# Kernel tuning notes

Measured on AMD Instinct MI355X. Metric: run time of the kernel, lower is better.

The kernel has to match this reference:

```python
import jax, jax.numpy as jnp
import numpy as np

N_NODES = 100000
N_EDGES = 1600000
N_GRAPHS = 64


def _sage(x, src, dst, Wl, bl, Wr):
    # SAGEConv (mean aggr): out = lin_l(mean_j x_j) + lin_r(x_i)
    msg = x[src]                                             # [E, F] gather
    s = jax.ops.segment_sum(msg, dst, num_segments=N_NODES)  # [N, F]
    cnt = jax.ops.segment_sum(jnp.ones((msg.shape[0],), x.dtype), dst,
                              num_segments=N_NODES)[:, None]
    mean = jnp.where(cnt > 0, s / jnp.maximum(cnt, 1.0), 0.0)
    return mean @ Wl + bl + x @ Wr


def setup_inputs() -> dict:
    key = jax.random.key(0)
    ks = jax.random.split(key, 12)
    sc = lambda f: 1.0 / np.sqrt(f)
    inp = {
        'x':   jax.random.normal(ks[0], (N_NODES, 32), jnp.float32),
        'Wl0': jax.random.normal(ks[1], (32, 64), jnp.float32) * sc(32),
        'bl0': jnp.zeros((64,), jnp.float32),
        'Wr0': jax.random.normal(ks[2], (32, 64), jnp.float32) * sc(32),
        'Wl1': jax.random.normal(ks[3], (64, 64), jnp.float32) * sc(64),
        'bl1': jnp.zeros((64,), jnp.float32),
        'Wr1': jax.random.normal(ks[4], (64, 64), jnp.float32) * sc(64),
        'Wl2': jax.random.normal(ks[5], (64, 64), jnp.float32) * sc(64),
        'bl2': jnp.zeros((64,), jnp.float32),
        'Wr2': jax.random.normal(ks[6], (64, 64), jnp.float32) * sc(64),
        'W_out': jax.random.normal(ks[7], (64, 8), jnp.float32) * sc(64),
        'b_out': jnp.zeros((8,), jnp.float32),
        'edge_index': jax.random.randint(ks[8], (2, N_EDGES), 0, N_NODES, jnp.int32),
        'batch': jnp.sort(jax.random.randint(ks[9], (N_NODES,), 0, N_GRAPHS, jnp.int32)),
    }
    return inp


def reference(x, Wl0, bl0, Wr0, Wl1, bl1, Wr1, Wl2, bl2, Wr2,
              W_out, b_out, edge_index, batch):
    src, dst = edge_index[0], edge_index[1]
    h = _sage(x, src, dst, Wl0, bl0, Wr0)
    h = _sage(h, src, dst, Wl1, bl1, Wr1)
    h = _sage(h, src, dst, Wl2, bl2, Wr2)
    pooled = jax.ops.segment_max(h, batch, num_segments=N_GRAPHS)  # [G, 64]
    logits = pooled @ W_out + b_out
    return jax.nn.log_softmax(logits, axis=-1)
```

## Files before the change

### kernel.cpp

```cpp
#include <hip/hip_runtime.h>
#include <math.h>
#include <stdint.h>

#define N_NODES 100000
#define N_EDGES 1600000
#define N_GRAPHS 64

#define BSH 9
#define NBKT 196
#define NCHUNK 256
#define EPC 6250
#define FLAT (NBKT * NCHUNK)


typedef __attribute__((ext_vector_type(8))) short bf16x8;
typedef __attribute__((ext_vector_type(8))) unsigned short u16x8;
typedef __attribute__((ext_vector_type(4))) float f32x4;

#define WT0L 0
#define WT0R 2048
#define WT1L 4096
#define WT1R 8192
#define WT2L 12288
#define WT2R 16384

__device__ __forceinline__ void atomicMaxFloat(float* addr, float val) {
    if (val >= 0.0f) {
        atomicMax((int*)addr, __float_as_int(val));
    } else {
        atomicMin((unsigned int*)addr, __float_as_uint(val));
    }
}

__device__ __forceinline__ unsigned short f2bf(float f) {
    unsigned u = __float_as_uint(f);
    unsigned r = (u + 0x7FFFu + ((u >> 16) & 1u)) >> 16;
    return (unsigned short)r;
}
__device__ __forceinline__ float bf2f(unsigned short b) {
    return __uint_as_float(((unsigned)b) << 16);
}

__global__ __launch_bounds__(256) void k_prep(
    const float* __restrict__ x, unsigned short* __restrict__ xhi,
    const int* __restrict__ batch, int* __restrict__ gstart,
    float* __restrict__ pooled,
    const float* __restrict__ Wl0, const float* __restrict__ Wr0,
    const float* __restrict__ Wl1, const float* __restrict__ Wr1,
    const float* __restrict__ Wl2, const float* __restrict__ Wr2,
    unsigned short* __restrict__ WT,
    const int* __restrict__ dst, int* __restrict__ S) {
    __shared__ int h[NBKT];
    int i = blockIdx.x * blockDim.x + threadIdx.x;

    if (i < N_NODES * 32 / 8) {
        int base = i * 8;
        const float4* xp = (const float4*)(x + base);
        float4 a = xp[0], b = xp[1];
        u16x8 o;
        o[0] = f2bf(a.x); o[1] = f2bf(a.y); o[2] = f2bf(a.z); o[3] = f2bf(a.w);
        o[4] = f2bf(b.x); o[5] = f2bf(b.y); o[6] = f2bf(b.z); o[7] = f2bf(b.w);
        *(u16x8*)(xhi + base) = o;
    }
    if (i < N_GRAPHS * 64) pooled[i] = -INFINITY;
    if (i < N_NODES) {
        int b = batch[i];
        if (i == 0) {
            for (int g = 0; g <= b; ++g) gstart[g] = 0;
        } else {
            int pb = batch[i - 1];
            for (int g = pb + 1; g <= b; ++g) gstart[g] = i;
        }
        if (i == N_NODES - 1) {
            for (int g = b + 1; g <= N_GRAPHS; ++g) gstart[g] = N_NODES;
        }
    }
    if (i < 2560) {
        const float* Wsrc; int wofs, KW, local;
        if (i < 256)       { Wsrc = Wl0; wofs = WT0L; KW = 32; local = i; }
        else if (i < 512)  { Wsrc = Wr0; wofs = WT0R; KW = 32; local = i - 256; }
        else if (i < 1024) { Wsrc = Wl1; wofs = WT1L; KW = 64; local = i - 512; }
        else if (i < 1536) { Wsrc = Wr1; wofs = WT1R; KW = 64; local = i - 1024; }
        else if (i < 2048) { Wsrc = Wl2; wofs = WT2L; KW = 64; local = i - 1536; }
        else               { Wsrc = Wr2; wofs = WT2R; KW = 64; local = i - 2048; }
        int e = local * 8;
        int colw = e / KW, k0 = e % KW;
        u16x8 o;
#pragma unroll
        for (int j = 0; j < 8; ++j) o[j] = f2bf(Wsrc[(size_t)(k0 + j) * 64 + colw]);
        *(u16x8*)(WT + wofs + e) = o;
    }
    if (blockIdx.x < NCHUNK) {
        for (int q = threadIdx.x; q < NBKT; q += 256) h[q] = 0;
        __syncthreads();
        int c = blockIdx.x;
        int e0 = c * EPC;
        for (int e = e0 + threadIdx.x; e < e0 + EPC; e += 256)
            atomicAdd(&h[dst[e] >> BSH], 1);
        __syncthreads();
        for (int q = threadIdx.x; q < NBKT; q += 256) S[q * NCHUNK + c] = h[q];
    }
}

__global__ __launch_bounds__(1024) void k_rscan(int* __restrict__ S) {
    __shared__ int part[1024];
    int t = threadIdx.x;
    const int seg = (FLAT + 1023) / 1024;
    int lo = t * seg;
    int hi = lo + seg; if (hi > FLAT) hi = FLAT;
    int s = 0;
    for (int i = lo; i < hi; ++i) s += S[i];
    part[t] = s;
    __syncthreads();
    for (int off = 1; off < 1024; off <<= 1) {
        int add = (t >= off) ? part[t - off] : 0;
        __syncthreads();
        part[t] += add;
        __syncthreads();
    }
    int ex = (t > 0) ? part[t - 1] : 0;
    if (t == 1023) S[FLAT] = part[1023];
    int run = ex;
    for (int i = lo; i < hi; ++i) { int v = S[i]; S[i] = run; run += v; }
}

__global__ __launch_bounds__(256) void k_rscatter(
    const int* __restrict__ src, const int* __restrict__ dst,
    const int* __restrict__ S, unsigned int* __restrict__ pairs) {
    __shared__ int ofs[NBKT];
    __shared__ int cnt[NBKT];
    int c = blockIdx.x;
    for (int i = threadIdx.x; i < NBKT; i += 256) {
        ofs[i] = S[i * NCHUNK + c];
        cnt[i] = 0;
    }
    __syncthreads();
    int e0 = c * EPC;
    for (int e = e0 + threadIdx.x; e < e0 + EPC; e += 256) {
        int d = dst[e];
        int b = d >> BSH;
        int r = atomicAdd(&cnt[b], 1);
        pairs[ofs[b] + r] = ((unsigned)(d & 511) << 17) | (unsigned)src[e];
    }
}

__global__ __launch_bounds__(256) void k_rbuild(
    const unsigned int* __restrict__ pairs, const int* __restrict__ S,
    int* __restrict__ row_ptr, int* __restrict__ col) {
    __shared__ int ncnt[512];
    __shared__ int nofs[512];
    __shared__ int part[256];
    int b = blockIdx.x;
    int t = threadIdx.x;
    int base = S[b * NCHUNK];
    int next = (b == NBKT - 1) ? S[FLAT] : S[(b + 1) * NCHUNK];
    int count = next - base;
    int nodeBase = b << BSH;

    ncnt[2 * t] = 0; ncnt[2 * t + 1] = 0;
    __syncthreads();
    for (int i = t; i < count; i += 256)
        atomicAdd(&ncnt[pairs[base + i] >> 17], 1);
    __syncthreads();
    int v0 = ncnt[2 * t], v1 = ncnt[2 * t + 1];
    part[t] = v0 + v1;
    __syncthreads();
    for (int off = 1; off < 256; off <<= 1) {
        int add = (t >= off) ? part[t - off] : 0;
        __syncthreads();
        part[t] += add;
        __syncthreads();
    }
    int ex = (t > 0) ? part[t - 1] : 0;
    nofs[2 * t] = ex;
    nofs[2 * t + 1] = ex + v0;
    ncnt[2 * t] = 0; ncnt[2 * t + 1] = 0;
    __syncthreads();
    for (int i = t; i < 512; i += 256) {
        int node = nodeBase + i;
        if (node < N_NODES) row_ptr[node] = base + nofs[i];
    }
    if (b == 0 && t == 0) row_ptr[N_NODES] = N_EDGES;
    for (int i = t; i < count; i += 256) {
        unsigned p = pairs[base + i];
        int li = p >> 17;
        int r = atomicAdd(&ncnt[li], 1);
        col[base + nofs[li] + r] = (int)(p & 0x1FFFFu);
    }
}

template <int KM, bool XBF, int KX, int XS, int OM>
__global__ __launch_bounds__(256) void k_sage_fused(
    const unsigned short* __restrict__ ghb,
    const float* x,
    const unsigned short* xhi, const unsigned short* xlo,
    const int* __restrict__ row_ptr, const int* __restrict__ col,
    const unsigned short* __restrict__ WTl,
    const float* __restrict__ bl,
    const unsigned short* __restrict__ WTr,
    unsigned short* ohi, unsigned short* olo) {
    __shared__ float amean[2][16][KM + 4];

    int lane = threadIdx.x & 63;
    int wid  = threadIdx.x >> 6;
    int sl   = wid >> 1;
    int half = wid & 1;
    int strip = blockIdx.x * 2 + sl;
    int row0 = strip * 16;

    {
        constexpr int G = (KM == 64) ? 4 : 8;
        constexpr int LPR = 64 / G;
        int g  = lane / LPR;
        int fq = lane % LPR;
        int nodeBase = row0 + half * 8;
        int rp = row_ptr[nodeBase + (lane < 8 ? lane : 8)];

        for (int i = 0; i < 8; ++i) {
            int start = __shfl(rp, i);
            int end   = __shfl(rp, i + 1);
            float s0 = 0.0f, s1 = 0.0f, s2 = 0.0f, s3 = 0.0f;

            for (int eb = start; eb < end; eb += 64) {
                int n = end - eb; if (n > 64) n = 64;
                int c = (eb + lane < end) ? col[eb + lane] : 0;
                int j = 0;
                for (; j + 4 * G - 1 < n; j += 4 * G) {
                    int cA = __shfl(c, j + g);
                    int cB = __shfl(c, j + G + g);
                    int cC = __shfl(c, j + 2 * G + g);
                    int cD = __shfl(c, j + 3 * G + g);
                    ushort4 vA = *(const ushort4*)(ghb + (size_t)cA * KM + fq * 4);
                    ushort4 vB = *(const ushort4*)(ghb + (size_t)cB * KM + fq * 4);
                    ushort4 vC = *(const ushort4*)(ghb + (size_t)cC * KM + fq * 4);
                    ushort4 vD = *(const ushort4*)(ghb + (size_t)cD * KM + fq * 4);
                    s0 += (bf2f(vA.x) + bf2f(vB.x)) + (bf2f(vC.x) + bf2f(vD.x));
                    s1 += (bf2f(vA.y) + bf2f(vB.y)) + (bf2f(vC.y) + bf2f(vD.y));
                    s2 += (bf2f(vA.z) + bf2f(vB.z)) + (bf2f(vC.z) + bf2f(vD.z));
                    s3 += (bf2f(vA.w) + bf2f(vB.w)) + (bf2f(vC.w) + bf2f(vD.w));
                }
                for (; j + 2 * G - 1 < n; j += 2 * G) {
                    int cA = __shfl(c, j + g);
                    int cB = __shfl(c, j + G + g);
                    ushort4 vA = *(const ushort4*)(ghb + (size_t)cA * KM + fq * 4);
                    ushort4 vB = *(const ushort4*)(ghb + (size_t)cB * KM + fq * 4);
                    s0 += bf2f(vA.x) + bf2f(vB.x);
                    s1 += bf2f(vA.y) + bf2f(vB.y);
                    s2 += bf2f(vA.z) + bf2f(vB.z);
                    s3 += bf2f(vA.w) + bf2f(vB.w);
                }
                for (; j + G - 1 < n; j += G) {
                    int cA = __shfl(c, j + g);
                    ushort4 vA = *(const ushort4*)(ghb + (size_t)cA * KM + fq * 4);
                    s0 += bf2f(vA.x);
                    s1 += bf2f(vA.y);
                    s2 += bf2f(vA.z);
                    s3 += bf2f(vA.w);
                }
                if (j < n) {
                    int idx = j + g;
                    bool valid = idx < n;
                    int cA = __shfl(c, valid ? idx : 0);
                    ushort4 vA = *(const ushort4*)(ghb + (size_t)cA * KM + fq * 4);
                    if (valid) {
                        s0 += bf2f(vA.x);
                        s1 += bf2f(vA.y);
                        s2 += bf2f(vA.z);
                        s3 += bf2f(vA.w);
                    }
                }
            }
#pragma unroll
            for (int m = LPR; m < 64; m <<= 1) {
                s0 += __shfl_xor(s0, m);
                s1 += __shfl_xor(s1, m);
                s2 += __shfl_xor(s2, m);
                s3 += __shfl_xor(s3, m);
            }
            int deg = end - start;
            float inv = (deg > 0) ? 1.0f / (float)deg : 0.0f;
            if (lane < LPR) {
                int lr = half * 8 + i;
                *(float4*)&amean[sl][lr][fq * 4] =
                    make_float4(s0 * inv, s1 * inv, s2 * inv, s3 * inv);
            }
        }
    }
    __syncthreads();

    int m = lane & 15;
    int g = lane >> 4;
    f32x4 acc[2] = {};

#pragma unroll
    for (int kt = 0; kt < KM / 32; ++kt) {
        int k0 = kt * 32 + g * 8;
        const float* ar = &amean[sl][m][k0];
        float4 a0 = *(const float4*)(ar);
        float4 a1 = *(const float4*)(ar + 4);
        float av[8] = {a0.x, a0.y, a0.z, a0.w, a1.x, a1.y, a1.z, a1.w};
        bf16x8 ahi, alo;
#pragma unroll
        for (int j = 0; j < 8; ++j) {
            unsigned short hb = f2bf(av[j]);
            ahi[j] = (short)hb;
            alo[j] = (short)f2bf(av[j] - bf2f(hb));
        }
#pragma unroll
        for (int nti = 0; nti < 2; ++nti) {
            int nt = half * 2 + nti;
            bf16x8 b = *(const bf16x8*)(WTl + (size_t)(nt * 16 + m) * KM + k0);
            acc[nti] = __builtin_amdgcn_mfma_f32_16x16x32_bf16(ahi, b, acc[nti], 0, 0, 0);
            acc[nti] = __builtin_amdgcn_mfma_f32_16x16x32_bf16(alo, b, acc[nti], 0, 0, 0);
        }
    }
#pragma unroll
    for (int kt = 0; kt < KX / 32; ++kt) {
        int k0 = kt * 32 + g * 8;
        bf16x8 ahi, alo;
        if constexpr (XBF) {
            ahi = *(const bf16x8*)(xhi + (size_t)(row0 + m) * XS + k0);
            alo = *(const bf16x8*)(xlo + (size_t)(row0 + m) * XS + k0);
        } else {
            const float4* ap = (const float4*)(x + (size_t)(row0 + m) * XS + k0);
            float4 a0 = ap[0], a1 = ap[1];
            float av[8] = {a0.x, a0.y, a0.z, a0.w, a1.x, a1.y, a1.z, a1.w};
#pragma unroll
            for (int j = 0; j < 8; ++j) {
                unsigned short hb = f2bf(av[j]);
                ahi[j] = (short)hb;
                alo[j] = (short)f2bf(av[j] - bf2f(hb));
            }
        }
#pragma unroll
        for (int nti = 0; nti < 2; ++nti) {
            int nt = half * 2 + nti;
            bf16x8 b = *(const bf16x8*)(WTr + (size_t)(nt * 16 + m) * KX + k0);
            acc[nti] = __builtin_amdgcn_mfma_f32_16x16x32_bf16(ahi, b, acc[nti], 0, 0, 0);
            acc[nti] = __builtin_amdgcn_mfma_f32_16x16x32_bf16(alo, b, acc[nti], 0, 0, 0);
        }
    }
#pragma unroll
    for (int nti = 0; nti < 2; ++nti) {
        int nt = half * 2 + nti;
        float bias = bl[nt * 16 + m];
#pragma unroll
        for (int r = 0; r < 4; ++r) {
            int row = row0 + g * 4 + r;
            float v = acc[nti][r] + bias;
            if constexpr (OM == 1) {
                unsigned short hb = f2bf(v);
                ohi[(size_t)row * 64 + nt * 16 + m] = hb;
                olo[(size_t)row * 64 + nt * 16 + m] = f2bf(v - bf2f(hb));
            } else {
                ohi[(size_t)row * 64 + nt * 16 + m] = f2bf(v);
            }
        }
    }
}

#define PSPLIT 8
__global__ __launch_bounds__(256) void k_pool2(const unsigned short* __restrict__ h,
                                               const int* __restrict__ gstart,
                                               float* __restrict__ pooled) {
    __shared__ float red[4][64];
    int gr = blockIdx.x & 63;
    int split = blockIdx.x >> 6;
    int lane = threadIdx.x & 63;
    int w = threadIdx.x >> 6;
    int s = gstart[gr], e = gstart[gr + 1];
    float m = -INFINITY;
    for (int i = s + split * 4 + w; i < e; i += PSPLIT * 4)
        m = fmaxf(m, bf2f(h[(size_t)i * 64 + lane]));
    red[w][lane] = m;
    __syncthreads();
    if (w == 0) {
        m = fmaxf(fmaxf(red[0][lane], red[1][lane]),
                  fmaxf(red[2][lane], red[3][lane]));
        if (m > -INFINITY) atomicMaxFloat(&pooled[gr * 64 + lane], m);
    }
}

__global__ void k_head(const float* __restrict__ pooled,
                       const float* __restrict__ Wout,
                       const float* __restrict__ bout, float* __restrict__ out) {
    int tid = threadIdx.x;
    int g = tid >> 3, o = tid & 7;
    float acc = bout[o];
#pragma unroll
    for (int k = 0; k < 64; ++k) acc += pooled[g * 64 + k] * Wout[k * 8 + o];
    float mx = acc;
#pragma unroll
    for (int m = 1; m < 8; m <<= 1) mx = fmaxf(mx, __shfl_xor(mx, m));
    float ex = expf(acc - mx);
    float sum = ex;
#pragma unroll
    for (int m = 1; m < 8; m <<= 1) sum += __shfl_xor(sum, m);
    out[g * 8 + o] = (acc - mx) - logf(sum);
}

extern "C" void kernel_launch(void* const* d_in, const int* in_sizes, int n_in,
                              void* d_out, int out_size, void* d_ws, size_t ws_size,
                              hipStream_t stream) {
    const float* x    = (const float*)d_in[0];
    const float* Wl0  = (const float*)d_in[1];
    const float* bl0  = (const float*)d_in[2];
    const float* Wr0  = (const float*)d_in[3];
    const float* Wl1  = (const float*)d_in[4];
    const float* bl1  = (const float*)d_in[5];
    const float* Wr1  = (const float*)d_in[6];
    const float* Wl2  = (const float*)d_in[7];
    const float* bl2  = (const float*)d_in[8];
    const float* Wr2  = (const float*)d_in[9];
    const float* Wout = (const float*)d_in[10];
    const float* bout = (const float*)d_in[11];
    const int*   eidx = (const int*)d_in[12];
    const int*   batch= (const int*)d_in[13];
    const int* src = eidx;
    const int* dst = eidx + N_EDGES;

    uint8_t* ws = (uint8_t*)d_ws;
    int*   S       = (int*)(ws + 0);
    unsigned short* WT = (unsigned short*)(ws + 204800);
    int*   row_ptr = (int*)(ws + 400128);
    int*   col     = (int*)(ws + 800256);
    float* pooled  = (float*)(ws + 7200384);
    int*   gstart  = (int*)(ws + 7216768);
    unsigned short* H1hi = (unsigned short*)(ws + 7217408);
    unsigned short* H1lo = (unsigned short*)(ws + 20017408);
    unsigned short* H2hi = (unsigned short*)(ws + 32817408);
    unsigned short* H2lo = (unsigned short*)(ws + 45617408);
    unsigned int* pairs  = (unsigned int*)(ws + 32817408);
    unsigned short* Xhi  = (unsigned short*)(ws + 45617408);

    k_prep<<<(N_NODES * 32 / 8 + 255) / 256, 256, 0, stream>>>(
        x, Xhi, batch, gstart, pooled,
        Wl0, Wr0, Wl1, Wr1, Wl2, Wr2, WT, dst, S);
    k_rscan<<<1, 1024, 0, stream>>>(S);
    k_rscatter<<<NCHUNK, 256, 0, stream>>>(src, dst, S, pairs);
    k_rbuild<<<NBKT, 256, 0, stream>>>(pairs, S, row_ptr, col);

    int fusedBlocks = N_NODES / 32;

    k_sage_fused<32, false, 32, 32, 1><<<fusedBlocks, 256, 0, stream>>>(
        Xhi, x, nullptr, nullptr, row_ptr, col,
        WT + WT0L, bl0, WT + WT0R, H1hi, H1lo);
    k_sage_fused<64, true, 64, 64, 1><<<fusedBlocks, 256, 0, stream>>>(
        H1hi, nullptr, H1hi, H1lo, row_ptr, col,
        WT + WT1L, bl1, WT + WT1R, H2hi, H2lo);
    k_sage_fused<64, true, 64, 64, 2><<<fusedBlocks, 256, 0, stream>>>(
        H2hi, nullptr, H2hi, H2lo, row_ptr, col,
        WT + WT2L, bl2, WT + WT2R, H1hi, nullptr);

    k_pool2<<<64 * PSPLIT, 256, 0, stream>>>(H1hi, gstart, pooled);
    k_head<<<1, 512, 0, stream>>>(pooled, Wout, bout, (float*)d_out);
}
```

Baseline: 222.8 us.

## Shrink fused SAGE block to one 16-row strip with four waves

Each block of the fused SAGE kernel now covers one 16-node strip instead of two. Each of the four waves gathers neighbour means for 4 nodes instead of 8, then computes a single 16-column output tile instead of two. The launch uses twice as many blocks, and each wave has a shorter serial gather chain and half the MFMA accumulators, which is meant to raise parallelism and latency hiding in the gather phase. In exchange there are more blocks and barriers, and the A operand is converted to hi/lo split in every wave with no reuse across two output tiles.

```diff
diff --git a/kernel.cpp b/kernel.cpp
--- a/kernel.cpp
+++ b/kernel.cpp
@@ -199,24 +199,21 @@
     const float* __restrict__ bl,
     const unsigned short* __restrict__ WTr,
     unsigned short* ohi, unsigned short* olo) {
-    __shared__ float amean[2][16][KM + 4];
+    __shared__ float amean[16][KM + 4];
 
     int lane = threadIdx.x & 63;
     int wid  = threadIdx.x >> 6;
-    int sl   = wid >> 1;
-    int half = wid & 1;
-    int strip = blockIdx.x * 2 + sl;
-    int row0 = strip * 16;
+    int row0 = blockIdx.x * 16;
 
     {
         constexpr int G = (KM == 64) ? 4 : 8;
         constexpr int LPR = 64 / G;
         int g  = lane / LPR;
         int fq = lane % LPR;
-        int nodeBase = row0 + half * 8;
-        int rp = row_ptr[nodeBase + (lane < 8 ? lane : 8)];
-
-        for (int i = 0; i < 8; ++i) {
+        int nodeBase = row0 + wid * 4;
+        int rp = row_ptr[nodeBase + (lane < 4 ? lane : 4)];
+
+        for (int i = 0; i < 4; ++i) {
             int start = __shfl(rp, i);
             int end   = __shfl(rp, i + 1);
             float s0 = 0.0f, s1 = 0.0f, s2 = 0.0f, s3 = 0.0f;
@@ -280,8 +277,8 @@
             int deg = end - start;
             float inv = (deg > 0) ? 1.0f / (float)deg : 0.0f;
             if (lane < LPR) {
-                int lr = half * 8 + i;
-                *(float4*)&amean[sl][lr][fq * 4] =
+                int lr = wid * 4 + i;
+                *(float4*)&amean[lr][fq * 4] =
                     make_float4(s0 * inv, s1 * inv, s2 * inv, s3 * inv);
             }
         }
@@ -290,12 +287,13 @@
 
     int m = lane & 15;
     int g = lane >> 4;
-    f32x4 acc[2] = {};
+    int nt = wid;
+    f32x4 acc = {};
 
 #pragma unroll
     for (int kt = 0; kt < KM / 32; ++kt) {
         int k0 = kt * 32 + g * 8;
-        const float* ar = &amean[sl][m][k0];
+        const float* ar = &amean[m][k0];
         float4 a0 = *(const float4*)(ar);
         float4 a1 = *(const float4*)(ar + 4);
         float av[8] = {a0.x, a0.y, a0.z, a0.w, a1.x, a1.y, a1.z, a1.w};
@@ -306,13 +304,9 @@
             ahi[j] = (short)hb;
             alo[j] = (short)f2bf(av[j] - bf2f(hb));
         }
-#pragma unroll
-        for (int nti = 0; nti < 2; ++nti) {
-            int nt = half * 2 + nti;
-            bf16x8 b = *(const bf16x8*)(WTl + (size_t)(nt * 16 + m) * KM + k0);
-            acc[nti] = __builtin_amdgcn_mfma_f32_16x16x32_bf16(ahi, b, acc[nti], 0, 0, 0);
-            acc[nti] = __builtin_amdgcn_mfma_f32_16x16x32_bf16(alo, b, acc[nti], 0, 0, 0);
-        }
+        bf16x8 b = *(const bf16x8*)(WTl + (size_t)(nt * 16 + m) * KM + k0);
+        acc = __builtin_amdgcn_mfma_f32_16x16x32_bf16(ahi, b, acc, 0, 0, 0);
+        acc = __builtin_amdgcn_mfma_f32_16x16x32_bf16(alo, b, acc, 0, 0, 0);
     }
 #pragma unroll
     for (int kt = 0; kt < KX / 32; ++kt) {
@@ -332,29 +326,21 @@
                 alo[j] = (short)f2bf(av[j] - bf2f(hb));
             }
         }
-#pragma unroll
-        for (int nti = 0; nti < 2; ++nti) {
-            int nt = half * 2 + nti;
-            bf16x8 b = *(const bf16x8*)(WTr + (size_t)(nt * 16 + m) * KX + k0);
-            acc[nti] = __builtin_amdgcn_mfma_f32_16x16x32_bf16(ahi, b, acc[nti], 0, 0, 0);
-            acc[nti] = __builtin_amdgcn_mfma_f32_16x16x32_bf16(alo, b, acc[nti], 0, 0, 0);
-        }
-    }
-#pragma unroll
-    for (int nti = 0; nti < 2; ++nti) {
-        int nt = half * 2 + nti;
-        float bias = bl[nt * 16 + m];
-#pragma unroll
-        for (int r = 0; r < 4; ++r) {
-            int row = row0 + g * 4 + r;
-            float v = acc[nti][r] + bias;
-            if constexpr (OM == 1) {
-                unsigned short hb = f2bf(v);
-                ohi[(size_t)row * 64 + nt * 16 + m] = hb;
-                olo[(size_t)row * 64 + nt * 16 + m] = f2bf(v - bf2f(hb));
-            } else {
-                ohi[(size_t)row * 64 + nt * 16 + m] = f2bf(v);
-            }
+        bf16x8 b = *(const bf16x8*)(WTr + (size_t)(nt * 16 + m) * KX + k0);
+        acc = __builtin_amdgcn_mfma_f32_16x16x32_bf16(ahi, b, acc, 0, 0, 0);
+        acc = __builtin_amdgcn_mfma_f32_16x16x32_bf16(alo, b, acc, 0, 0, 0);
+    }
+    float bias = bl[nt * 16 + m];
+#pragma unroll
+    for (int r = 0; r < 4; ++r) {
+        int row = row0 + g * 4 + r;
+        float v = acc[r] + bias;
+        if constexpr (OM == 1) {
+            unsigned short hb = f2bf(v);
+            ohi[(size_t)row * 64 + nt * 16 + m] = hb;
+            olo[(size_t)row * 64 + nt * 16 + m] = f2bf(v - bf2f(hb));
+        } else {
+            ohi[(size_t)row * 64 + nt * 16 + m] = f2bf(v);
         }
     }
 }
@@ -440,7 +426,7 @@
     k_rscatter<<<NCHUNK, 256, 0, stream>>>(src, dst, S, pairs);
     k_rbuild<<<NBKT, 256, 0, stream>>>(pairs, S, row_ptr, col);
 
-    int fusedBlocks = N_NODES / 32;
+    int fusedBlocks = N_NODES / 16;
 
     k_sage_fused<32, false, 32, 32, 1><<<fusedBlocks, 256, 0, stream>>>(
         Xhi, x, nullptr, nullptr, row_ptr, col,
```

Result: slower. 230.8 us (+3.6%).
